# Optimization experiments

Measured on AMD Instinct MI355X. Metric: run time of the kernel, lower is better.

Reference implementation:

```python
import jax, jax.numpy as jnp
import numpy as np

ITERS = 3

def squash(s, axis):
    # v = (|s|^2 / (1 + |s|^2)) * s / |s|
    sn = jnp.sum(s * s, axis=axis, keepdims=True)
    return sn / (1.0 + sn) * s / jnp.sqrt(sn)

def setup_inputs() -> dict:
    key = jax.random.key(0)
    k1, k2 = jax.random.split(key)
    b, B, C, P2, f = 8, 144, 16, 16, 12
    u = jax.random.normal(k1, (b, B, C, P2, f, f), dtype=jnp.float32)
    a = jax.random.uniform(k2, (b, B, f, f), dtype=jnp.float32)
    return {"u": u, "a": a}

def reference(u, a):
    # u: (b, B, C, P2, f, f); a: (b, B, f, f)
    b, B, C, P2, f, _ = u.shape
    # r: (b, B, C, 1, f, f), initialized uniform over C scaled by activation
    r = jnp.broadcast_to(a[:, :, None, None, :, :] * (1.0 / C), (b, B, C, 1, f, f))
    v = None
    for i in range(ITERS):
        c = jax.nn.softmax(r, axis=2)                       # over C
        v = squash(jnp.sum(c * u, axis=1, keepdims=True), axis=3)  # (b,1,C,P2,f,f)
        if i != ITERS - 1:
            r = r + jnp.sum(u * v, axis=3, keepdims=True)   # agreement over psize
    a_out = jnp.sqrt(jnp.sum(v * v, axis=3, keepdims=True))  # (b,1,C,1,f,f)
    return (jnp.squeeze(v, axis=1), jnp.squeeze(a_out, axis=(1, 3)))
```

## Files before the change

### kernel.cpp

```cpp
#include <hip/hip_runtime.h>
#include <math.h>


#define NB 8
#define BDIM 144
#define CDIM 16
#define PDIM 16
#define SDIM 144
#define PT 16
#define BC 8
#define NPT (SDIM / PT)
#define NBC (BDIM / BC)
#define USTRIDE (CDIM * PDIM * SDIM)
#define VELEMS (NB * CDIM * PDIM * SDIM)
#define AELEMS (NB * CDIM * SDIM)


__global__ __launch_bounds__(256) void s0_kernel(const float* __restrict__ u,
                                                 float* __restrict__ part) {
  const int o = blockIdx.x * 256 + threadIdx.x;
  const int chunk = blockIdx.y;
  const int q4 = o % 36;
  const int t1 = o / 36;
  const int p = t1 & 15;
  const int t2 = t1 >> 4;
  const int c = t2 & 15;
  const int b = t2 >> 4;

  const float4* ub = (const float4*)(u +
      ((size_t)((b * BDIM + chunk * BC) * CDIM + c) * PDIM + p) * SDIM) + q4;
  float sx = 0.f, sy = 0.f, sz = 0.f, sw = 0.f;
#pragma unroll
  for (int j = 0; j < BC; ++j) {
    const float4 v = ub[(size_t)j * (USTRIDE / 4)];
    sx += v.x; sy += v.y; sz += v.z; sw += v.w;
  }
  const float sc = 1.0f / CDIM;
  float4* sp = (float4*)(part + (size_t)chunk * VELEMS +
                         ((size_t)((b * CDIM + c) * PDIM + p)) * SDIM) + q4;
  *sp = make_float4(sx * sc, sy * sc, sz * sc, sw * sc);
}

__global__ __launch_bounds__(256) void sP_kernel(const float* __restrict__ u,
                                                 const float* __restrict__ a,
                                                 const float* __restrict__ V,
                                                 float* __restrict__ part) {
  __shared__ float Vt[CDIM][PDIM][PT + 1];
  __shared__ float ebuf[2][CDIM][PT + 1];
  __shared__ float atile[BC][PT];

  const int tid = threadIdx.x;
  const int pos = tid & 15;
  const int c = tid >> 4;
  const int b = blockIdx.z;
  const int posg = blockIdx.y * PT + pos;
  const int B0 = blockIdx.x * BC;

  const float* ubase =
      u + ((size_t)((b * BDIM + B0) * CDIM + c) * PDIM) * SDIM + posg;

  {
    const int vb = ((b * CDIM + c) * PDIM) * SDIM + posg;
#pragma unroll
    for (int p = 0; p < PDIM; ++p) Vt[c][p][pos] = V[vb + p * SDIM];
    if (tid < BC * PT) {
      const int j = tid >> 4;
      atile[j][pos] =
          a[(b * BDIM + B0 + j) * SDIM + blockIdx.y * PT + pos] * (1.0f / CDIM);
    }
  }
  __syncthreads();

  float sacc[PDIM];
#pragma unroll
  for (int p = 0; p < PDIM; ++p) sacc[p] = 0.f;

  float uvbuf[2][PDIM];
#pragma unroll
  for (int p = 0; p < PDIM; ++p) uvbuf[0][p] = ubase[p * SDIM];

#pragma unroll
  for (int j = 0; j < BC; ++j) {
    float* uv = uvbuf[j & 1];
    float* uvn = uvbuf[(j + 1) & 1];
    if (j + 1 < BC) {
      const float* ub = ubase + (size_t)(j + 1) * USTRIDE;
#pragma unroll
      for (int p = 0; p < PDIM; ++p) uvn[p] = ub[p * SDIM];
    }
    float dot = 0.f;
#pragma unroll
    for (int p = 0; p < PDIM; ++p) dot += uv[p] * Vt[c][p][pos];
    const float e = __expf(atile[j][pos] + dot);
    ebuf[j & 1][c][pos] = e;
    __syncthreads();
    float sum = 0.f;
#pragma unroll
    for (int c2 = 0; c2 < CDIM; ++c2) sum += ebuf[j & 1][c2][pos];
    const float w = e * __builtin_amdgcn_rcpf(sum);
#pragma unroll
    for (int p = 0; p < PDIM; ++p) sacc[p] += w * uv[p];
  }

  float* sp = part + (size_t)blockIdx.x * VELEMS +
              ((b * CDIM + c) * PDIM) * SDIM + posg;
#pragma unroll
  for (int p = 0; p < PDIM; ++p) sp[p * SDIM] = sacc[p];
}

__global__ __launch_bounds__(256) void qP_kernel(const float* __restrict__ part,
                                                 float* __restrict__ V,
                                                 float* __restrict__ out_v,
                                                 float* __restrict__ out_a,
                                                 int iter) {
  const int gid = blockIdx.x * 256 + threadIdx.x;
  const int b = gid / (CDIM * SDIM);
  const int rem = gid - b * (CDIM * SDIM);
  const int c = rem / SDIM;
  const int posg = rem - c * SDIM;
  const int base = ((b * CDIM + c) * PDIM) * SDIM + posg;

  float sv[PDIM];
#pragma unroll
  for (int p = 0; p < PDIM; ++p) sv[p] = 0.f;
#pragma unroll
  for (int k = 0; k < NBC; ++k) {
    const float* sp = part + (size_t)k * VELEMS + base;
#pragma unroll
    for (int p = 0; p < PDIM; ++p) sv[p] += sp[p * SDIM];
  }
  float sn = 0.f;
#pragma unroll
  for (int p = 0; p < PDIM; ++p) sn += sv[p] * sv[p];
  const float scale = sn / (1.0f + sn) * rsqrtf(sn);

  if (iter == 0) {
#pragma unroll
    for (int p = 0; p < PDIM; ++p) V[base + p * SDIM] = sv[p] * scale;
  } else if (iter == 1) {
#pragma unroll
    for (int p = 0; p < PDIM; ++p) V[base + p * SDIM] += sv[p] * scale;
  } else {
    float vv = 0.f;
#pragma unroll
    for (int p = 0; p < PDIM; ++p) {
      const float v = sv[p] * scale;
      out_v[base + p * SDIM] = v;
      vv += v * v;
    }
    out_a[gid] = sqrtf(vv);
  }
}


__global__ __launch_bounds__(256) void s_kernel(const float* __restrict__ u,
                                                const float* __restrict__ a,
                                                const float* __restrict__ V,
                                                float* __restrict__ s,
                                                int iter) {
  __shared__ float Vt[CDIM][PDIM][PT];
  __shared__ float ebuf[2][CDIM][PT + 1];
  __shared__ float atile[BC][PT];

  const int tid = threadIdx.x;
  const int pos = tid & 15;
  const int c = tid >> 4;
  const int b = blockIdx.z;
  const int posg = blockIdx.y * PT + pos;
  const int B0 = blockIdx.x * BC;

  const float* ubase =
      u + ((size_t)((b * BDIM + B0) * CDIM + c) * PDIM) * SDIM + posg;

  float sacc[PDIM];
#pragma unroll
  for (int p = 0; p < PDIM; ++p) sacc[p] = 0.f;

  if (iter == 0) {
#pragma unroll 2
    for (int j = 0; j < BC; ++j) {
      const float* ub = ubase + (size_t)j * USTRIDE;
#pragma unroll
      for (int p = 0; p < PDIM; ++p) sacc[p] += ub[p * SDIM];
    }
    const int sb = ((b * CDIM + c) * PDIM) * SDIM + posg;
#pragma unroll
    for (int p = 0; p < PDIM; ++p)
      atomicAdd(&s[sb + p * SDIM], sacc[p] * (1.0f / CDIM));
    return;
  }

  {
    const int vb = ((b * CDIM + c) * PDIM) * SDIM + posg;
#pragma unroll
    for (int p = 0; p < PDIM; ++p) Vt[c][p][pos] = V[vb + p * SDIM];
    if (tid < BC * PT) {
      const int j = tid >> 4;
      atile[j][pos] =
          a[(b * BDIM + B0 + j) * SDIM + blockIdx.y * PT + pos] * (1.0f / CDIM);
    }
  }
  __syncthreads();

  float uvbuf[2][PDIM];
#pragma unroll
  for (int p = 0; p < PDIM; ++p) uvbuf[0][p] = ubase[p * SDIM];

#pragma unroll
  for (int j = 0; j < BC; ++j) {
    float* uv = uvbuf[j & 1];
    float* uvn = uvbuf[(j + 1) & 1];
    if (j + 1 < BC) {
      const float* ub = ubase + (size_t)(j + 1) * USTRIDE;
#pragma unroll
      for (int p = 0; p < PDIM; ++p) uvn[p] = ub[p * SDIM];
    }
    float dot = 0.f;
#pragma unroll
    for (int p = 0; p < PDIM; ++p) dot += uv[p] * Vt[c][p][pos];
    const float e = __expf(atile[j][pos] + dot);
    ebuf[j & 1][c][pos] = e;
    __syncthreads();
    float sum = 0.f;
#pragma unroll
    for (int c2 = 0; c2 < CDIM; ++c2) sum += ebuf[j & 1][c2][pos];
    const float w = e * __builtin_amdgcn_rcpf(sum);
#pragma unroll
    for (int p = 0; p < PDIM; ++p) sacc[p] += w * uv[p];
  }

  const int sb = ((b * CDIM + c) * PDIM) * SDIM + posg;
#pragma unroll
  for (int p = 0; p < PDIM; ++p) atomicAdd(&s[sb + p * SDIM], sacc[p]);
}

__global__ __launch_bounds__(256) void q_kernel(float* __restrict__ s,
                                                float* __restrict__ V,
                                                float* __restrict__ out_v,
                                                float* __restrict__ out_a,
                                                int iter) {
  const int gid = blockIdx.x * 256 + threadIdx.x;
  const int b = gid / (CDIM * SDIM);
  const int rem = gid - b * (CDIM * SDIM);
  const int c = rem / SDIM;
  const int posg = rem - c * SDIM;
  const int base = ((b * CDIM + c) * PDIM) * SDIM + posg;

  float sv[PDIM];
  float sn = 0.f;
#pragma unroll
  for (int p = 0; p < PDIM; ++p) {
    const float x = s[base + p * SDIM];
    sv[p] = x;
    sn += x * x;
  }
  const float scale = sn / (1.0f + sn) * rsqrtf(sn);

  if (iter < 2) {
#pragma unroll
    for (int p = 0; p < PDIM; ++p) {
      V[base + p * SDIM] += sv[p] * scale;
      s[base + p * SDIM] = 0.f;
    }
  } else {
    float vv = 0.f;
#pragma unroll
    for (int p = 0; p < PDIM; ++p) {
      const float v = sv[p] * scale;
      out_v[base + p * SDIM] = v;
      vv += v * v;
    }
    out_a[gid] = sqrtf(vv);
  }
}


extern "C" void kernel_launch(void* const* d_in, const int* in_sizes, int n_in,
                              void* d_out, int out_size, void* d_ws, size_t ws_size,
                              hipStream_t stream) {
  const float* u = (const float*)d_in[0];
  const float* a = (const float*)d_in[1];
  float* out_v = (float*)d_out;
  float* out_a = out_v + VELEMS;
  float* V = (float*)d_ws;

  const size_t needP = (size_t)(1 + NBC) * VELEMS * sizeof(float);
  if (ws_size >= needP) {
    float* part = V + VELEMS;
    const dim3 gS(NBC, NPT, NB);
    for (int it = 0; it < 3; ++it) {
      if (it == 0)
        s0_kernel<<<dim3(VELEMS / 4 / 256, NBC), 256, 0, stream>>>(u, part);
      else
        sP_kernel<<<gS, 256, 0, stream>>>(u, a, V, part);
      qP_kernel<<<AELEMS / 256, 256, 0, stream>>>(part, V, out_v, out_a, it);
    }
  } else {
    float* s = V + VELEMS;
    hipMemsetAsync(d_ws, 0, (size_t)2 * VELEMS * sizeof(float), stream);
    const dim3 gS(NBC, NPT, NB);
    for (int it = 0; it < 3; ++it) {
      s_kernel<<<gS, 256, 0, stream>>>(u, a, V, s, it);
      q_kernel<<<AELEMS / 256, 256, 0, stream>>>(s, V, out_v, out_a, it);
    }
  }
}
```

Measured before the change: 356.2 us.

## Fuse routing partial sums and squash via last-block counter into one kernel

Merges the per-chunk routing kernel and the squash/reduce kernel into a single kernel. Each (batch, position-tile) group counts finished blocks with an atomic counter, and the last block to finish reduces the partials and applies squash. This removes three kernel launches and the separate reduction pass. In exchange the reduction runs on only one block per group, serialised behind the last arrival, which may limit parallelism in the squash step. The per-step __syncthreads is also replaced with an explicit LDS waitcnt plus a raw barrier, and the fallback path for small workspaces is dropped.

```diff
diff --git a/kernel.cpp b/kernel.cpp
--- a/kernel.cpp
+++ b/kernel.cpp
@@ -14,116 +14,107 @@
 #define USTRIDE (CDIM * PDIM * SDIM)
 #define VELEMS (NB * CDIM * PDIM * SDIM)
 #define AELEMS (NB * CDIM * SDIM)
+#define NGROUP (NB * NPT)
 
-
-__global__ __launch_bounds__(256) void s0_kernel(const float* __restrict__ u,
-                                                 float* __restrict__ part) {
-  const int o = blockIdx.x * 256 + threadIdx.x;
-  const int chunk = blockIdx.y;
-  const int q4 = o % 36;
-  const int t1 = o / 36;
-  const int p = t1 & 15;
-  const int t2 = t1 >> 4;
-  const int c = t2 & 15;
-  const int b = t2 >> 4;
-
-  const float4* ub = (const float4*)(u +
-      ((size_t)((b * BDIM + chunk * BC) * CDIM + c) * PDIM + p) * SDIM) + q4;
-  float sx = 0.f, sy = 0.f, sz = 0.f, sw = 0.f;
-#pragma unroll
-  for (int j = 0; j < BC; ++j) {
-    const float4 v = ub[(size_t)j * (USTRIDE / 4)];
-    sx += v.x; sy += v.y; sz += v.z; sw += v.w;
-  }
-  const float sc = 1.0f / CDIM;
-  float4* sp = (float4*)(part + (size_t)chunk * VELEMS +
-                         ((size_t)((b * CDIM + c) * PDIM + p)) * SDIM) + q4;
-  *sp = make_float4(sx * sc, sy * sc, sz * sc, sw * sc);
-}
-
-__global__ __launch_bounds__(256) void sP_kernel(const float* __restrict__ u,
-                                                 const float* __restrict__ a,
-                                                 const float* __restrict__ V,
-                                                 float* __restrict__ part) {
+__global__ __launch_bounds__(256) void route_kernel(
+    const float* __restrict__ u, const float* __restrict__ a,
+    float* __restrict__ V, float* __restrict__ part,
+    unsigned int* __restrict__ cnt,
+    float* __restrict__ out_v, float* __restrict__ out_a, int iter) {
   __shared__ float Vt[CDIM][PDIM][PT + 1];
   __shared__ float ebuf[2][CDIM][PT + 1];
   __shared__ float atile[BC][PT];
+  __shared__ int isLast;
 
   const int tid = threadIdx.x;
   const int pos = tid & 15;
   const int c = tid >> 4;
+  const int chunk = blockIdx.x;
+  const int y = blockIdx.y;
   const int b = blockIdx.z;
-  const int posg = blockIdx.y * PT + pos;
-  const int B0 = blockIdx.x * BC;
+  const int posg = y * PT + pos;
+  const int B0 = chunk * BC;
 
   const float* ubase =
       u + ((size_t)((b * BDIM + B0) * CDIM + c) * PDIM) * SDIM + posg;
-
-  {
-    const int vb = ((b * CDIM + c) * PDIM) * SDIM + posg;
-#pragma unroll
-    for (int p = 0; p < PDIM; ++p) Vt[c][p][pos] = V[vb + p * SDIM];
-    if (tid < BC * PT) {
-      const int j = tid >> 4;
-      atile[j][pos] =
-          a[(b * BDIM + B0 + j) * SDIM + blockIdx.y * PT + pos] * (1.0f / CDIM);
-    }
-  }
-  __syncthreads();
 
   float sacc[PDIM];
 #pragma unroll
   for (int p = 0; p < PDIM; ++p) sacc[p] = 0.f;
 
-  float uvbuf[2][PDIM];
+  if (iter == 0) {
+#pragma unroll 2
+    for (int j = 0; j < BC; ++j) {
+      const float* ub = ubase + (size_t)j * USTRIDE;
 #pragma unroll
-  for (int p = 0; p < PDIM; ++p) uvbuf[0][p] = ubase[p * SDIM];
+      for (int p = 0; p < PDIM; ++p) sacc[p] += ub[p * SDIM];
+    }
+#pragma unroll
+    for (int p = 0; p < PDIM; ++p) sacc[p] *= (1.0f / CDIM);
+  } else {
+    float uvbuf[2][PDIM];
+#pragma unroll
+    for (int p = 0; p < PDIM; ++p) uvbuf[0][p] = ubase[p * SDIM];
+
+    {
+      const int vb = ((b * CDIM + c) * PDIM) * SDIM + posg;
+#pragma unroll
+      for (int p = 0; p < PDIM; ++p) Vt[c][p][pos] = V[vb + p * SDIM];
+      if (tid < BC * PT) {
+        const int j = tid >> 4;
+        atile[j][pos] =
+            a[(b * BDIM + B0 + j) * SDIM + y * PT + pos] * (1.0f / CDIM);
+      }
+    }
+    __syncthreads();
 
 #pragma unroll
-  for (int j = 0; j < BC; ++j) {
-    float* uv = uvbuf[j & 1];
-    float* uvn = uvbuf[(j + 1) & 1];
-    if (j + 1 < BC) {
-      const float* ub = ubase + (size_t)(j + 1) * USTRIDE;
+    for (int j = 0; j < BC; ++j) {
+      float* uv = uvbuf[j & 1];
+      float* uvn = uvbuf[(j + 1) & 1];
+      if (j + 1 < BC) {
+        const float* ub = ubase + (size_t)(j + 1) * USTRIDE;
 #pragma unroll
-      for (int p = 0; p < PDIM; ++p) uvn[p] = ub[p * SDIM];
+        for (int p = 0; p < PDIM; ++p) uvn[p] = ub[p * SDIM];
+      }
+      float dot = 0.f;
+#pragma unroll
+      for (int p = 0; p < PDIM; ++p) dot += uv[p] * Vt[c][p][pos];
+      const float e = __expf(atile[j][pos] + dot);
+      ebuf[j & 1][c][pos] = e;
+      asm volatile("s_waitcnt lgkmcnt(0)" ::: "memory");
+      __builtin_amdgcn_s_barrier();
+      float sum = 0.f;
+#pragma unroll
+      for (int c2 = 0; c2 < CDIM; ++c2) sum += ebuf[j & 1][c2][pos];
+      const float w = e * __builtin_amdgcn_rcpf(sum);
+#pragma unroll
+      for (int p = 0; p < PDIM; ++p) sacc[p] += w * uv[p];
     }
-    float dot = 0.f;
-#pragma unroll
-    for (int p = 0; p < PDIM; ++p) dot += uv[p] * Vt[c][p][pos];
-    const float e = __expf(atile[j][pos] + dot);
-    ebuf[j & 1][c][pos] = e;
-    __syncthreads();
-    float sum = 0.f;
-#pragma unroll
-    for (int c2 = 0; c2 < CDIM; ++c2) sum += ebuf[j & 1][c2][pos];
-    const float w = e * __builtin_amdgcn_rcpf(sum);
-#pragma unroll
-    for (int p = 0; p < PDIM; ++p) sacc[p] += w * uv[p];
   }
 
-  float* sp = part + (size_t)blockIdx.x * VELEMS +
-              ((b * CDIM + c) * PDIM) * SDIM + posg;
+  {
+    float* sp = part + (size_t)chunk * VELEMS +
+                ((b * CDIM + c) * PDIM) * SDIM + posg;
 #pragma unroll
-  for (int p = 0; p < PDIM; ++p) sp[p * SDIM] = sacc[p];
-}
+    for (int p = 0; p < PDIM; ++p) sp[p * SDIM] = sacc[p];
+  }
 
-__global__ __launch_bounds__(256) void qP_kernel(const float* __restrict__ part,
-                                                 float* __restrict__ V,
-                                                 float* __restrict__ out_v,
-                                                 float* __restrict__ out_a,
-                                                 int iter) {
-  const int gid = blockIdx.x * 256 + threadIdx.x;
-  const int b = gid / (CDIM * SDIM);
-  const int rem = gid - b * (CDIM * SDIM);
-  const int c = rem / SDIM;
-  const int posg = rem - c * SDIM;
-  const int base = ((b * CDIM + c) * PDIM) * SDIM + posg;
+  __threadfence();
+  __syncthreads();
+  if (tid == 0) {
+    const unsigned old = atomicAdd(&cnt[iter * NGROUP + b * NPT + y], 1u);
+    isLast = (old == (NBC - 1));
+  }
+  __syncthreads();
+  if (!isLast) return;
+  __threadfence();
 
   float sv[PDIM];
 #pragma unroll
   for (int p = 0; p < PDIM; ++p) sv[p] = 0.f;
-#pragma unroll
+  const int base = ((b * CDIM + c) * PDIM) * SDIM + posg;
+#pragma unroll 2
   for (int k = 0; k < NBC; ++k) {
     const float* sp = part + (size_t)k * VELEMS + base;
 #pragma unroll
@@ -148,129 +139,7 @@
       out_v[base + p * SDIM] = v;
       vv += v * v;
     }
-    out_a[gid] = sqrtf(vv);
-  }
-}
-
-
-__global__ __launch_bounds__(256) void s_kernel(const float* __restrict__ u,
-                                                const float* __restrict__ a,
-                                                const float* __restrict__ V,
-                                                float* __restrict__ s,
-                                                int iter) {
-  __shared__ float Vt[CDIM][PDIM][PT];
-  __shared__ float ebuf[2][CDIM][PT + 1];
-  __shared__ float atile[BC][PT];
-
-  const int tid = threadIdx.x;
-  const int pos = tid & 15;
-  const int c = tid >> 4;
-  const int b = blockIdx.z;
-  const int posg = blockIdx.y * PT + pos;
-  const int B0 = blockIdx.x * BC;
-
-  const float* ubase =
-      u + ((size_t)((b * BDIM + B0) * CDIM + c) * PDIM) * SDIM + posg;
-
-  float sacc[PDIM];
-#pragma unroll
-  for (int p = 0; p < PDIM; ++p) sacc[p] = 0.f;
-
-  if (iter == 0) {
-#pragma unroll 2
-    for (int j = 0; j < BC; ++j) {
-      const float* ub = ubase + (size_t)j * USTRIDE;
-#pragma unroll
-      for (int p = 0; p < PDIM; ++p) sacc[p] += ub[p * SDIM];
-    }
-    const int sb = ((b * CDIM + c) * PDIM) * SDIM + posg;
-#pragma unroll
-    for (int p = 0; p < PDIM; ++p)
-      atomicAdd(&s[sb + p * SDIM], sacc[p] * (1.0f / CDIM));
-    return;
-  }
-
-  {
-    const int vb = ((b * CDIM + c) * PDIM) * SDIM + posg;
-#pragma unroll
-    for (int p = 0; p < PDIM; ++p) Vt[c][p][pos] = V[vb + p * SDIM];
-    if (tid < BC * PT) {
-      const int j = tid >> 4;
-      atile[j][pos] =
-          a[(b * BDIM + B0 + j) * SDIM + blockIdx.y * PT + pos] * (1.0f / CDIM);
-    }
-  }
-  __syncthreads();
-
-  float uvbuf[2][PDIM];
-#pragma unroll
-  for (int p = 0; p < PDIM; ++p) uvbuf[0][p] = ubase[p * SDIM];
-
-#pragma unroll
-  for (int j = 0; j < BC; ++j) {
-    float* uv = uvbuf[j & 1];
-    float* uvn = uvbuf[(j + 1) & 1];
-    if (j + 1 < BC) {
-      const float* ub = ubase + (size_t)(j + 1) * USTRIDE;
-#pragma unroll
-      for (int p = 0; p < PDIM; ++p) uvn[p] = ub[p * SDIM];
-    }
-    float dot = 0.f;
-#pragma unroll
-    for (int p = 0; p < PDIM; ++p) dot += uv[p] * Vt[c][p][pos];
-    const float e = __expf(atile[j][pos] + dot);
-    ebuf[j & 1][c][pos] = e;
-    __syncthreads();
-    float sum = 0.f;
-#pragma unroll
-    for (int c2 = 0; c2 < CDIM; ++c2) sum += ebuf[j & 1][c2][pos];
-    const float w = e * __builtin_amdgcn_rcpf(sum);
-#pragma unroll
-    for (int p = 0; p < PDIM; ++p) sacc[p] += w * uv[p];
-  }
-
-  const int sb = ((b * CDIM + c) * PDIM) * SDIM + posg;
-#pragma unroll
-  for (int p = 0; p < PDIM; ++p) atomicAdd(&s[sb + p * SDIM], sacc[p]);
-}
-
-__global__ __launch_bounds__(256) void q_kernel(float* __restrict__ s,
-                                                float* __restrict__ V,
-                                                float* __restrict__ out_v,
-                                                float* __restrict__ out_a,
-                                                int iter) {
-  const int gid = blockIdx.x * 256 + threadIdx.x;
-  const int b = gid / (CDIM * SDIM);
-  const int rem = gid - b * (CDIM * SDIM);
-  const int c = rem / SDIM;
-  const int posg = rem - c * SDIM;
-  const int base = ((b * CDIM + c) * PDIM) * SDIM + posg;
-
-  float sv[PDIM];
-  float sn = 0.f;
-#pragma unroll
-  for (int p = 0; p < PDIM; ++p) {
-    const float x = s[base + p * SDIM];
-    sv[p] = x;
-    sn += x * x;
-  }
-  const float scale = sn / (1.0f + sn) * rsqrtf(sn);
-
-  if (iter < 2) {
-#pragma unroll
-    for (int p = 0; p < PDIM; ++p) {
-      V[base + p * SDIM] += sv[p] * scale;
-      s[base + p * SDIM] = 0.f;
-    }
-  } else {
-    float vv = 0.f;
-#pragma unroll
-    for (int p = 0; p < PDIM; ++p) {
-      const float v = sv[p] * scale;
-      out_v[base + p * SDIM] = v;
-      vv += v * v;
-    }
-    out_a[gid] = sqrtf(vv);
+    out_a[(b * CDIM + c) * SDIM + posg] = sqrtf(vv);
   }
 }
 
@@ -282,26 +151,14 @@
   const float* a = (const float*)d_in[1];
   float* out_v = (float*)d_out;
   float* out_a = out_v + VELEMS;
+
   float* V = (float*)d_ws;
+  float* part = V + VELEMS;
+  unsigned int* cnt = (unsigned int*)(part + (size_t)NBC * VELEMS);
 
-  const size_t needP = (size_t)(1 + NBC) * VELEMS * sizeof(float);
-  if (ws_size >= needP) {
-    float* part = V + VELEMS;
-    const dim3 gS(NBC, NPT, NB);
-    for (int it = 0; it < 3; ++it) {
-      if (it == 0)
-        s0_kernel<<<dim3(VELEMS / 4 / 256, NBC), 256, 0, stream>>>(u, part);
-      else
-        sP_kernel<<<gS, 256, 0, stream>>>(u, a, V, part);
-      qP_kernel<<<AELEMS / 256, 256, 0, stream>>>(part, V, out_v, out_a, it);
-    }
-  } else {
-    float* s = V + VELEMS;
-    hipMemsetAsync(d_ws, 0, (size_t)2 * VELEMS * sizeof(float), stream);
-    const dim3 gS(NBC, NPT, NB);
-    for (int it = 0; it < 3; ++it) {
-      s_kernel<<<gS, 256, 0, stream>>>(u, a, V, s, it);
-      q_kernel<<<AELEMS / 256, 256, 0, stream>>>(s, V, out_v, out_a, it);
-    }
-  }
+  hipMemsetAsync(cnt, 0, 3 * NGROUP * sizeof(unsigned int), stream);
+
+  const dim3 g(NBC, NPT, NB);
+  for (int it = 0; it < 3; ++it)
+    route_kernel<<<g, 256, 0, stream>>>(u, a, V, part, cnt, out_v, out_a, it);
 }
```

Result: slower. 1.158 ms (+225.1%).
